# Performance work log

Hardware: AMD Instinct MI355X
Metric: run time of the kernel (lower is better)

The kernel has to match this reference:

```python
import jax, jax.numpy as jnp
import numpy as np

N_NODES = 100000


def _spmm(edge_index, edge_weight, x):
    # out[i] = sum_j A[i, j] * x[j]; row=dst=edge_index[0], col=src=edge_index[1]
    dst, src = edge_index[0], edge_index[1]
    msgs = edge_weight[:, None] * x[src]  # [E, d]
    return jax.ops.segment_sum(msgs, dst, num_segments=N_NODES)


def setup_inputs() -> dict:
    key = jax.random.key(0)
    k1, k2, k3, k4 = jax.random.split(key, 4)
    N, E, D = N_NODES, 3200000, 64
    features = jax.random.normal(k1, (N, D), dtype=jnp.float32)
    edge_weight = jax.random.uniform(k2, (E,), dtype=jnp.float32)
    dst = jax.random.randint(k3, (E,), 0, N)
    src = jax.random.randint(k4, (E,), 0, N)
    edge_index = jnp.stack([dst, src]).astype(jnp.int64)
    return {"features": features, "edge_weight": edge_weight,
            "edge_index": edge_index, "degree": 2}


def reference(features, edge_weight, edge_index, degree):
    # SGC: features = adj @ features, repeated `degree` times (no learned params)
    x = features
    for _ in range(degree):
        x = _spmm(edge_index, edge_weight, x)
    return x
```

## Files before the change

kernel.cpp:

```cpp
#include <hip/hip_runtime.h>
#include <hip/hip_fp16.h>

#define N_NODES 100000
#define DFEAT 64
#define NBK 782
#define NPB 128
#define CAPB 4608
#define CPAD 16
#define SPAN 12500

__device__ __forceinline__ void scan2_1024(int v0, int v1, int* sb, int tid,
                                           int* e0, int* e1, int* total)
{
    __syncthreads();
    const int lane = tid & 63, wid = tid >> 6;
    int s = v0 + v1;
    int inc = s;
#pragma unroll
    for (int o = 1; o < 64; o <<= 1) {
        int t = __shfl_up(inc, o, 64);
        if (lane >= o) inc += t;
    }
    if (lane == 63) sb[wid] = inc;
    __syncthreads();
    if (wid == 0) {
        int wv = (lane < 8) ? sb[lane] : 0;
        int winc = wv;
#pragma unroll
        for (int o = 1; o < 8; o <<= 1) {
            int t = __shfl_up(winc, o, 64);
            if (lane >= o) winc += t;
        }
        if (lane < 8) sb[8 + lane] = winc - wv;
    }
    __syncthreads();
    int base = sb[8 + wid] + inc - s;
    *e0 = base;
    *e1 = base + v0;
    *total = sb[15] + sb[7];
}

__global__ __launch_bounds__(512) void sort_span(
    const int* __restrict__ dst, const int* __restrict__ src,
    const float* __restrict__ w,
    int* __restrict__ gcur,
    unsigned* __restrict__ recs_b,
    unsigned char* __restrict__ dloc_b,
    int E,
    const float* __restrict__ feat_in, __half* __restrict__ feat_out, int n2)
{
    __shared__ unsigned      lrec[SPAN];
    __shared__ unsigned char ldl[SPAN];
    __shared__ int hist[NBK];
    __shared__ int offL[NBK];
    __shared__ int cursL[NBK];
    __shared__ int runL[NBK];
    __shared__ int sb[16];

    const int base = blockIdx.x * SPAN;
    const int n    = min(SPAN, E - base);
    const int tid  = threadIdx.x;

    for (int i = tid; i < NBK; i += 512) hist[i] = 0;
    __syncthreads();

    for (int k = tid; k < n; k += 512) atomicAdd(&hist[dst[base + k] >> 7], 1);
    __syncthreads();

    const int i0 = 2 * tid, i1 = i0 + 1;
    int v0 = (i0 < NBK) ? hist[i0] : 0;
    int v1 = (i1 < NBK) ? hist[i1] : 0;
    int e0, e1, tot;
    scan2_1024(v0, v1, sb, tid, &e0, &e1, &tot);
    if (i0 < NBK) { offL[i0] = e0; cursL[i0] = e0; }
    if (i1 < NBK) { offL[i1] = e1; cursL[i1] = e1; }
    __syncthreads();

    for (int i = tid; i < NBK; i += 512) {
        int h = hist[i];
        runL[i] = h ? atomicAdd(&gcur[i * CPAD], h) : 0;
    }
    __syncthreads();

    for (int k = tid; k < n; k += 512) {
        int d = dst[base + k];
        int b = d >> 7;
        int pos = atomicAdd(&cursL[b], 1);
        unsigned wq = (unsigned)__float2int_rn(w[base + k] * 32768.0f);
        if (wq > 32767u) wq = 32767u;
        lrec[pos] = (unsigned)src[base + k] | (wq << 17);
        ldl[pos]  = (unsigned char)(d & 127);
    }
    __syncthreads();

    const int grp = tid >> 4;
    const int gl  = tid & 15;
    for (int c = grp; c < NBK; c += 32) {
        int off = offL[c];
        int L   = hist[c];
        int rb  = runL[c];
        const size_t gp0 = (size_t)c * CAPB;
        for (int k = gl; k < L; k += 16) {
            int p = rb + k;
            if (p < CAPB) {
                recs_b[gp0 + p] = lrec[off + k];
                dloc_b[gp0 + p] = ldl[off + k];
            }
        }
    }

    const int gstride = gridDim.x * 512;
    for (int i = blockIdx.x * 512 + tid; i < n2; i += gstride) {
        float2 f = ((const float2*)feat_in)[i];
        ((__half2*)feat_out)[i] = __floats2half2_rn(f.x, f.y);
    }
}

__global__ __launch_bounds__(512) void scan_buckets(
    const int* __restrict__ gcur, int* __restrict__ gbase,
    int* __restrict__ row_ptr, int E)
{
    __shared__ int sb[16];
    const int tid = threadIdx.x;
    const int i0 = 2 * tid, i1 = 2 * tid + 1;
    int v0 = (i0 < NBK) ? gcur[i0 * CPAD] : 0;
    int v1 = (i1 < NBK) ? gcur[i1 * CPAD] : 0;
    int e0, e1, tot;
    scan2_1024(v0, v1, sb, tid, &e0, &e1, &tot);
    if (i0 < NBK) gbase[i0] = e0;
    if (i1 < NBK) gbase[i1] = e1;
    if (tid == 0) row_ptr[N_NODES] = E;
}

__global__ __launch_bounds__(512) void finalize_csr(
    const int* __restrict__ gcur, const int* __restrict__ gbase,
    const unsigned* __restrict__ recs_b, const unsigned char* __restrict__ dloc_b,
    unsigned* __restrict__ edges_s, int* __restrict__ row_ptr)
{
    __shared__ unsigned      lrecL[CAPB];
    __shared__ unsigned char dlocL[CAPB];
    __shared__ int histL[NPB];
    __shared__ int cursorL[NPB];
    __shared__ int sb[16];

    const int b   = blockIdx.x;
    const int tid = threadIdx.x;
    const int cnt = min(gcur[b * CPAD], CAPB);
    const int gb  = gbase[b];

    if (tid < NPB) histL[tid] = 0;
    __syncthreads();

    const size_t rb = (size_t)b * CAPB;
    for (int k = tid; k < cnt; k += 512) {
        lrecL[k] = recs_b[rb + k];
        dlocL[k] = dloc_b[rb + k];
    }
    __syncthreads();

    for (int k = tid; k < cnt; k += 512) atomicAdd(&histL[dlocL[k]], 1);
    __syncthreads();

    int h0 = (2 * tid < NPB) ? histL[2 * tid] : 0;
    int h1 = (2 * tid + 1 < NPB) ? histL[2 * tid + 1] : 0;
    int he0, he1, htot;
    scan2_1024(h0, h1, sb, tid, &he0, &he1, &htot);
    if (2 * tid < NPB) {
        int i = b * NPB + 2 * tid;
        if (i < N_NODES) row_ptr[i] = gb + he0;
        cursorL[2 * tid] = gb + he0;
    }
    if (2 * tid + 1 < NPB) {
        int i = b * NPB + 2 * tid + 1;
        if (i < N_NODES) row_ptr[i] = gb + he1;
        cursorL[2 * tid + 1] = gb + he1;
    }
    __syncthreads();

    for (int k = tid; k < cnt; k += 512) {
        int pos = atomicAdd(&cursorL[dlocL[k]], 1);
        edges_s[pos] = lrecL[k];
    }
}

template <int OUT_FP16>
__global__ __launch_bounds__(256) void spmm_csr(
    const int* __restrict__ row_ptr,
    const unsigned* __restrict__ edges,
    const uint2* __restrict__ x4,
    void* __restrict__ outv)
{
    int node = __builtin_amdgcn_readfirstlane(blockIdx.x * 4 + (int)(threadIdx.x >> 6));
    if (node >= N_NODES) return;
    const int lane = threadIdx.x & 63;
    const int g    = lane >> 4;
    const int gl   = lane & 15;

    const int beg = row_ptr[node];
    const int end = row_ptr[node + 1];

    float a0 = 0.f, a1 = 0.f, a2 = 0.f, a3 = 0.f;
    int e0 = beg;
    const int nblk = (end - beg) >> 4;

#define ACC4(v, w) do {                                            \
        __half2 _h0 = *(__half2*)&(v).x;                           \
        __half2 _h1 = *(__half2*)&(v).y;                           \
        a0 += (w) * __low2float(_h0);  a1 += (w) * __high2float(_h0); \
        a2 += (w) * __low2float(_h1);  a3 += (w) * __high2float(_h1); \
    } while (0)

    if (nblk > 0) {
        unsigned n0 = edges[e0 +  0 + g];
        unsigned n1 = edges[e0 +  4 + g];
        unsigned n2 = edges[e0 +  8 + g];
        unsigned n3 = edges[e0 + 12 + g];
        e0 += 16;

        for (int b = 0; b < nblk; ++b) {
            uint2 v0 = x4[(size_t)(n0 & 0x1FFFF) * 16 + gl];
            uint2 v1 = x4[(size_t)(n1 & 0x1FFFF) * 16 + gl];
            uint2 v2 = x4[(size_t)(n2 & 0x1FFFF) * 16 + gl];
            uint2 v3 = x4[(size_t)(n3 & 0x1FFFF) * 16 + gl];

            float w0 = (float)(n0 >> 17), w1 = (float)(n1 >> 17);
            float w2 = (float)(n2 >> 17), w3 = (float)(n3 >> 17);

            if (b + 1 < nblk) {
                n0 = edges[e0 +  0 + g];
                n1 = edges[e0 +  4 + g];
                n2 = edges[e0 +  8 + g];
                n3 = edges[e0 + 12 + g];
                e0 += 16;
            }

            ACC4(v0, w0);
            ACC4(v1, w1);
            ACC4(v2, w2);
            ACC4(v3, w3);
        }
    }

    for (; e0 + 4 <= end; e0 += 4) {
        unsigned r = edges[e0 + g];
        uint2 v = x4[(size_t)(r & 0x1FFFF) * 16 + gl];
        float w = (float)(r >> 17);
        ACC4(v, w);
    }
    {
        int rem = end - e0;
        if (g < rem) {
            unsigned r = edges[e0 + g];
            uint2 v = x4[(size_t)(r & 0x1FFFF) * 16 + gl];
            float w = (float)(r >> 17);
            ACC4(v, w);
        }
    }
#undef ACC4

    a0 += __shfl_xor(a0, 16, 64);  a0 += __shfl_xor(a0, 32, 64);
    a1 += __shfl_xor(a1, 16, 64);  a1 += __shfl_xor(a1, 32, 64);
    a2 += __shfl_xor(a2, 16, 64);  a2 += __shfl_xor(a2, 32, 64);
    a3 += __shfl_xor(a3, 16, 64);  a3 += __shfl_xor(a3, 32, 64);

    if (g == 0) {
        const float k = 1.0f / 32768.0f;
        float s0 = a0 * k, s1 = a1 * k, s2 = a2 * k, s3 = a3 * k;
        if (OUT_FP16) {
            __half2 p0 = __floats2half2_rn(s0, s1);
            __half2 p1 = __floats2half2_rn(s2, s3);
            uint2 pv;
            pv.x = *(unsigned*)&p0;
            pv.y = *(unsigned*)&p1;
            ((uint2*)outv)[(size_t)node * 16 + gl] = pv;
        } else {
            ((float4*)outv)[(size_t)node * 16 + gl] = make_float4(s0, s1, s2, s3);
        }
    }
}

extern "C" void kernel_launch(void* const* d_in, const int* in_sizes, int n_in,
                              void* d_out, int out_size, void* d_ws, size_t ws_size,
                              hipStream_t stream) {
    const float* features = (const float*)d_in[0];
    const float* edge_w   = (const float*)d_in[1];
    const int*   edge_idx = (const int*)d_in[2];

    const int E = in_sizes[1];
    const int* dst = edge_idx;
    const int* src = edge_idx + E;

    const int nblkK1 = (E + SPAN - 1) / SPAN;

    char* ws = (char*)d_ws;
    unsigned*      recs_b  = (unsigned*)ws;      ws += (size_t)NBK * CAPB * sizeof(unsigned);
    unsigned char* dloc_b  = (unsigned char*)ws; ws += (size_t)NBK * CAPB;
    unsigned*      edges_s = (unsigned*)ws;      ws += (size_t)E * sizeof(unsigned);
    __half*        feat_h  = (__half*)ws;        ws += (size_t)N_NODES * DFEAT * sizeof(__half);
    int*           gcur    = (int*)ws;           ws += (size_t)NBK * CPAD * sizeof(int);
    int*           gbase   = (int*)ws;           ws += (size_t)NBK * sizeof(int);
    int*           row_ptr = (int*)ws;           ws += (size_t)(N_NODES + 1) * sizeof(int);

    __half* tmp_h = (__half*)recs_b;

    float* out = (float*)d_out;

    const int n2 = N_NODES * DFEAT / 2;

    hipMemsetAsync(gcur, 0, (size_t)NBK * CPAD * sizeof(int), stream);
    sort_span   <<<nblkK1, 512, 0, stream>>>(dst, src, edge_w, gcur, recs_b, dloc_b,
                                             E, features, feat_h, n2);
    scan_buckets<<<1, 512, 0, stream>>>(gcur, gbase, row_ptr, E);
    finalize_csr<<<NBK, 512, 0, stream>>>(gcur, gbase, recs_b, dloc_b, edges_s, row_ptr);

    const int ngrid = (N_NODES + 3) / 4;
    spmm_csr<1><<<ngrid, 256, 0, stream>>>(row_ptr, edges_s, (const uint2*)feat_h, tmp_h);
    spmm_csr<0><<<ngrid, 256, 0, stream>>>(row_ptr, edges_s, (const uint2*)tmp_h, out);
}
```

Baseline: 294.5 us.

## Halve bucketing span, unroll scatter loops 4x, narrow copy groups to 8 lanes

Halves the per-block edge span so the bucketing kernel launches twice as many blocks. The histogram, scatter, fp16 conversion and local-sort loops are manually unrolled by four so several independent global loads are in flight before the LDS atomics. The per-bucket copy-out now uses 8-lane groups, matching the smaller per-block bucket sizes. More blocks mean more global cursor atomics and shorter coalesced runs when copying out.

```diff
diff --git a/kernel.cpp b/kernel.cpp
--- a/kernel.cpp
+++ b/kernel.cpp
@@ -7,7 +7,7 @@
 #define NPB 128
 #define CAPB 4608
 #define CPAD 16
-#define SPAN 12500
+#define SPAN 6250
 
 __device__ __forceinline__ void scan2_1024(int v0, int v1, int* sb, int tid,
                                            int* e0, int* e1, int* total)
@@ -64,7 +64,20 @@
     for (int i = tid; i < NBK; i += 512) hist[i] = 0;
     __syncthreads();
 
-    for (int k = tid; k < n; k += 512) atomicAdd(&hist[dst[base + k] >> 7], 1);
+    {
+        int k = tid;
+        for (; k + 1536 < n; k += 2048) {
+            int d0 = dst[base + k];
+            int d1 = dst[base + k + 512];
+            int d2 = dst[base + k + 1024];
+            int d3 = dst[base + k + 1536];
+            atomicAdd(&hist[d0 >> 7], 1);
+            atomicAdd(&hist[d1 >> 7], 1);
+            atomicAdd(&hist[d2 >> 7], 1);
+            atomicAdd(&hist[d3 >> 7], 1);
+        }
+        for (; k < n; k += 512) atomicAdd(&hist[dst[base + k] >> 7], 1);
+    }
     __syncthreads();
 
     const int i0 = 2 * tid, i1 = i0 + 1;
@@ -82,25 +95,42 @@
     }
     __syncthreads();
 
-    for (int k = tid; k < n; k += 512) {
-        int d = dst[base + k];
-        int b = d >> 7;
-        int pos = atomicAdd(&cursL[b], 1);
-        unsigned wq = (unsigned)__float2int_rn(w[base + k] * 32768.0f);
-        if (wq > 32767u) wq = 32767u;
-        lrec[pos] = (unsigned)src[base + k] | (wq << 17);
-        ldl[pos]  = (unsigned char)(d & 127);
-    }
-    __syncthreads();
-
-    const int grp = tid >> 4;
-    const int gl  = tid & 15;
-    for (int c = grp; c < NBK; c += 32) {
+#define PROC(dv, sv, wv) do {                                       \
+        int _b = (dv) >> 7;                                         \
+        int _pos = atomicAdd(&cursL[_b], 1);                        \
+        unsigned _wq = (unsigned)__float2int_rn((wv) * 32768.0f);   \
+        if (_wq > 32767u) _wq = 32767u;                             \
+        lrec[_pos] = (unsigned)(sv) | (_wq << 17);                  \
+        ldl[_pos]  = (unsigned char)((dv) & 127);                   \
+    } while (0)
+    {
+        int k = tid;
+        for (; k + 1536 < n; k += 2048) {
+            int d0 = dst[base + k],        d1 = dst[base + k + 512];
+            int d2 = dst[base + k + 1024], d3 = dst[base + k + 1536];
+            int s0 = src[base + k],        s1 = src[base + k + 512];
+            int s2 = src[base + k + 1024], s3 = src[base + k + 1536];
+            float w0 = w[base + k],        w1 = w[base + k + 512];
+            float w2 = w[base + k + 1024], w3 = w[base + k + 1536];
+            PROC(d0, s0, w0); PROC(d1, s1, w1);
+            PROC(d2, s2, w2); PROC(d3, s3, w3);
+        }
+        for (; k < n; k += 512) {
+            int d = dst[base + k];
+            PROC(d, src[base + k], w[base + k]);
+        }
+    }
+#undef PROC
+    __syncthreads();
+
+    const int grp = tid >> 3;
+    const int gl  = tid & 7;
+    for (int c = grp; c < NBK; c += 64) {
         int off = offL[c];
         int L   = hist[c];
         int rb  = runL[c];
         const size_t gp0 = (size_t)c * CAPB;
-        for (int k = gl; k < L; k += 16) {
+        for (int k = gl; k < L; k += 8) {
             int p = rb + k;
             if (p < CAPB) {
                 recs_b[gp0 + p] = lrec[off + k];
@@ -109,10 +139,23 @@
         }
     }
 
-    const int gstride = gridDim.x * 512;
-    for (int i = blockIdx.x * 512 + tid; i < n2; i += gstride) {
-        float2 f = ((const float2*)feat_in)[i];
-        ((__half2*)feat_out)[i] = __floats2half2_rn(f.x, f.y);
+    {
+        const int gstride = gridDim.x * 512;
+        int i = blockIdx.x * 512 + tid;
+        for (; i + 3 * gstride < n2; i += 4 * gstride) {
+            float2 f0 = ((const float2*)feat_in)[i];
+            float2 f1 = ((const float2*)feat_in)[i + gstride];
+            float2 f2 = ((const float2*)feat_in)[i + 2 * gstride];
+            float2 f3 = ((const float2*)feat_in)[i + 3 * gstride];
+            ((__half2*)feat_out)[i]               = __floats2half2_rn(f0.x, f0.y);
+            ((__half2*)feat_out)[i + gstride]     = __floats2half2_rn(f1.x, f1.y);
+            ((__half2*)feat_out)[i + 2 * gstride] = __floats2half2_rn(f2.x, f2.y);
+            ((__half2*)feat_out)[i + 3 * gstride] = __floats2half2_rn(f3.x, f3.y);
+        }
+        for (; i < n2; i += gstride) {
+            float2 f = ((const float2*)feat_in)[i];
+            ((__half2*)feat_out)[i] = __floats2half2_rn(f.x, f.y);
+        }
     }
 }
 
@@ -152,13 +195,39 @@
     __syncthreads();
 
     const size_t rb = (size_t)b * CAPB;
-    for (int k = tid; k < cnt; k += 512) {
-        lrecL[k] = recs_b[rb + k];
-        dlocL[k] = dloc_b[rb + k];
-    }
-    __syncthreads();
-
-    for (int k = tid; k < cnt; k += 512) atomicAdd(&histL[dlocL[k]], 1);
+    {
+        int k = tid;
+        for (; k + 1536 < cnt; k += 2048) {
+            unsigned r0 = recs_b[rb + k];
+            unsigned r1 = recs_b[rb + k + 512];
+            unsigned r2 = recs_b[rb + k + 1024];
+            unsigned r3 = recs_b[rb + k + 1536];
+            unsigned char c0 = dloc_b[rb + k];
+            unsigned char c1 = dloc_b[rb + k + 512];
+            unsigned char c2 = dloc_b[rb + k + 1024];
+            unsigned char c3 = dloc_b[rb + k + 1536];
+            lrecL[k] = r0;        dlocL[k] = c0;
+            lrecL[k + 512] = r1;  dlocL[k + 512] = c1;
+            lrecL[k + 1024] = r2; dlocL[k + 1024] = c2;
+            lrecL[k + 1536] = r3; dlocL[k + 1536] = c3;
+        }
+        for (; k < cnt; k += 512) {
+            lrecL[k] = recs_b[rb + k];
+            dlocL[k] = dloc_b[rb + k];
+        }
+    }
+    __syncthreads();
+
+    {
+        int k = tid;
+        for (; k + 1536 < cnt; k += 2048) {
+            int a0 = dlocL[k], a1 = dlocL[k + 512];
+            int a2 = dlocL[k + 1024], a3 = dlocL[k + 1536];
+            atomicAdd(&histL[a0], 1); atomicAdd(&histL[a1], 1);
+            atomicAdd(&histL[a2], 1); atomicAdd(&histL[a3], 1);
+        }
+        for (; k < cnt; k += 512) atomicAdd(&histL[dlocL[k]], 1);
+    }
     __syncthreads();
 
     int h0 = (2 * tid < NPB) ? histL[2 * tid] : 0;
@@ -177,9 +246,24 @@
     }
     __syncthreads();
 
-    for (int k = tid; k < cnt; k += 512) {
-        int pos = atomicAdd(&cursorL[dlocL[k]], 1);
-        edges_s[pos] = lrecL[k];
+    {
+        int k = tid;
+        for (; k + 1536 < cnt; k += 2048) {
+            int a0 = dlocL[k];        unsigned r0 = lrecL[k];
+            int a1 = dlocL[k + 512];  unsigned r1 = lrecL[k + 512];
+            int a2 = dlocL[k + 1024]; unsigned r2 = lrecL[k + 1024];
+            int a3 = dlocL[k + 1536]; unsigned r3 = lrecL[k + 1536];
+            int p0 = atomicAdd(&cursorL[a0], 1);
+            int p1 = atomicAdd(&cursorL[a1], 1);
+            int p2 = atomicAdd(&cursorL[a2], 1);
+            int p3 = atomicAdd(&cursorL[a3], 1);
+            edges_s[p0] = r0; edges_s[p1] = r1;
+            edges_s[p2] = r2; edges_s[p3] = r3;
+        }
+        for (; k < cnt; k += 512) {
+            int pos = atomicAdd(&cursorL[dlocL[k]], 1);
+            edges_s[pos] = lrecL[k];
+        }
     }
 }
 
```

Measured after the change: 277.3 us. 5.8% less time.
